# Optimization experiments

Measured on AMD Instinct MI355X. Metric: run time of the kernel, lower is better.

## Reference

```python
import jax, jax.numpy as jnp
import numpy as np

N_NODES = 100000
N_EDGES = 1600000
D_FEAT = 256
HIDDEN = 256
OUT = 128


def _glorot(key, shape):
    fan_in, fan_out = shape[1], shape[0]
    lim = float(np.sqrt(6.0 / (fan_in + fan_out)))
    return jax.random.uniform(key, shape, jnp.float32, -lim, lim)


def setup_inputs() -> dict:
    key = jax.random.key(0)
    ks = jax.random.split(key, 12)
    x = jax.random.normal(ks[0], (N_NODES, D_FEAT), jnp.float32)
    edge_index = jax.random.randint(ks[1], (2, N_EDGES), 0, N_NODES, jnp.int64)
    return {
        "x": x,
        "edge_index": edge_index,
        # SAGEConv1: lin_l (neighbors, has bias), lin_r (root, no bias)
        "W1l": _glorot(ks[2], (HIDDEN, D_FEAT)),
        "b1l": jnp.zeros((HIDDEN,), jnp.float32),
        "W1r": _glorot(ks[3], (HIDDEN, D_FEAT)),
        # SAGEConv2
        "W2l": _glorot(ks[4], (OUT, HIDDEN)),
        "b2l": jnp.zeros((OUT,), jnp.float32),
        "W2r": _glorot(ks[5], (OUT, HIDDEN)),
        # EdgeDecoder
        "Wd1": _glorot(ks[6], (OUT, 2 * OUT)),
        "bd1": jnp.zeros((OUT,), jnp.float32),
        "Wd2": _glorot(ks[7], (1, OUT)),
        "bd2": jnp.zeros((1,), jnp.float32),
    }


def _sage_conv(x, src, dst, Wl, bl, Wr):
    # mean-aggregate source features into destination nodes (PyG SAGEConv, aggr='mean')
    msg_sum = jax.ops.segment_sum(x[src], dst, num_segments=N_NODES)  # [N, d]
    cnt = jax.ops.segment_sum(jnp.ones((src.shape[0],), x.dtype), dst, num_segments=N_NODES)
    mean = msg_sum / jnp.maximum(cnt, 1.0)[:, None]
    return mean @ Wl.T + bl + x @ Wr.T


def reference(x, edge_index, W1l, b1l, W1r, W2l, b2l, W2r, Wd1, bd1, Wd2, bd2):
    src, dst = edge_index[0], edge_index[1]
    # NodeEncoder
    h = jax.nn.relu(_sage_conv(x, src, dst, W1l, b1l, W1r))
    z = _sage_conv(h, src, dst, W2l, b2l, W2r)  # [N, OUT]
    # EdgeDecoder: gather per-edge endpoint embeddings, concat, MLP
    zc = jnp.concatenate([z[src], z[dst]], axis=-1)  # [E, 2*OUT]
    hd = jax.nn.relu(zc @ Wd1.T + bd1)
    out = hd @ Wd2.T + bd2  # [E, 1]
    return out.reshape(-1)
```

## Files before the change

kernel.cpp:

```cpp
#include <hip/hip_runtime.h>
#include <stdint.h>

static constexpr int NN = 100000;
static constexpr int NE = 1600000;
static constexpr int NB_SCAN = (NN + 255) / 256;
static constexpr int NB_CVTX = NN * 256 / 4 / 256;
static constexpr int NB_HIST = NE / 256;
static constexpr int NB_CVTW = 897;

typedef __bf16 bf16;
typedef __bf16 bf16x4 __attribute__((ext_vector_type(4)));
typedef __bf16 bf16x8 __attribute__((ext_vector_type(8)));
typedef float floatx4 __attribute__((ext_vector_type(4)));

__device__ __forceinline__ void async16(const void* g, void* l) {
  __builtin_amdgcn_global_load_lds(
      (const __attribute__((address_space(1))) void*)g,
      (__attribute__((address_space(3))) void*)l, 16, 0, 0);
}

__device__ __forceinline__ uint32_t pk4_fp8(float a, float b, float c, float d) {
  uint32_t v = 0;
  v = (uint32_t)__builtin_amdgcn_cvt_pk_fp8_f32(a, b, (int)v, false);
  v = (uint32_t)__builtin_amdgcn_cvt_pk_fp8_f32(c, d, (int)v, true);
  return v;
}

__device__ __forceinline__ void acc_fp8x8(float* a, uint2 v) {
  a[0] += __builtin_amdgcn_cvt_f32_fp8(v.x, 0);
  a[1] += __builtin_amdgcn_cvt_f32_fp8(v.x, 1);
  a[2] += __builtin_amdgcn_cvt_f32_fp8(v.x, 2);
  a[3] += __builtin_amdgcn_cvt_f32_fp8(v.x, 3);
  a[4] += __builtin_amdgcn_cvt_f32_fp8(v.y, 0);
  a[5] += __builtin_amdgcn_cvt_f32_fp8(v.y, 1);
  a[6] += __builtin_amdgcn_cvt_f32_fp8(v.y, 2);
  a[7] += __builtin_amdgcn_cvt_f32_fp8(v.y, 3);
}

__device__ __forceinline__ int clampN(int c) {
  return ((unsigned)c < (unsigned)NN) ? c : 0;
}

__global__ void k_cvtx_hist(const float* __restrict__ x, bf16* __restrict__ xb,
                            uint32_t* __restrict__ xq,
                            const int* __restrict__ dst, int* __restrict__ cnt8,
                            uint16_t* __restrict__ rank) {
  int b = blockIdx.x;
  int m = b % 5;
  if (m < 4) {
    int cb = (b / 5) * 4 + m;
    int t = cb * 256 + threadIdx.x;
    const float4 v = ((const float4*)x)[t];
    bf16x4 o;
    o.x = (bf16)v.x; o.y = (bf16)v.y; o.z = (bf16)v.z; o.w = (bf16)v.w;
    ((bf16x4*)xb)[t] = o;
    xq[t] = pk4_fp8(v.x, v.y, v.z, v.w);
  } else {
    int hb = b / 5;
    int e = hb * 256 + threadIdx.x;
    uint32_t xcd;
    asm("s_getreg_b32 %0, hwreg(HW_REG_XCC_ID)" : "=s"(xcd));
    xcd &= 7u;
    int d = dst[e];
    int old = __hip_atomic_fetch_add(&cnt8[(size_t)xcd * NN + d], 1,
                                     __ATOMIC_RELAXED, __HIP_MEMORY_SCOPE_WORKGROUP);
    rank[e] = (uint16_t)((xcd << 12) | ((uint32_t)old & 0xFFFu));
  }
}

__global__ void k_cvtw_scanpart(
    const float* __restrict__ W1l, const float* __restrict__ W1r,
    const float* __restrict__ W2l, const float* __restrict__ W2r,
    const float* __restrict__ Wd1, const float* __restrict__ bd1,
    bf16* __restrict__ B1, bf16* __restrict__ B2,
    bf16* __restrict__ Bd, float* __restrict__ biasPQ,
    const int* __restrict__ cnt8, int* __restrict__ part, int N) {
  int b = blockIdx.x;
  if (b < NB_CVTW) {
    int g = b * 256 + threadIdx.x;
    if (g < 131072) {
      int o = g >> 9, k = g & 511;
      float v = (k < 256) ? W1l[o * 256 + k] : W1r[o * 256 + k - 256];
      B1[g] = (bf16)v;
    } else if (g < 131072 + 65536) {
      int t = g - 131072;
      int o = t >> 8, k = t & 255;
      float v = (o < 128) ? W2l[o * 256 + k] : W2r[(o - 128) * 256 + k];
      B2[t] = (bf16)v;
    } else if (g < 131072 + 65536 + 32768) {
      int t = g - 196608;
      int o = t >> 7, k = t & 127;
      float v = (o < 128) ? Wd1[o * 256 + k] : Wd1[(o - 128) * 256 + 128 + k];
      Bd[t] = (bf16)v;
    } else if (g < 131072 + 65536 + 32768 + 256) {
      int t = g - 229376;
      biasPQ[t] = (t < 128) ? bd1[t] : 0.0f;
    }
  } else {
    __shared__ int sh[256];
    int bb = b - NB_CVTW;
    int t = threadIdx.x;
    int i = bb * 256 + t;
    int tot = 0;
    if (i < N) {
#pragma unroll
      for (int xx = 0; xx < 8; ++xx) tot += cnt8[(size_t)xx * NN + i];
    }
    sh[t] = tot;
    __syncthreads();
    for (int off = 128; off > 0; off >>= 1) {
      if (t < off) sh[t] += sh[t + off];
      __syncthreads();
    }
    if (t == 0) part[bb] = sh[0];
  }
}

__global__ __launch_bounds__(512) void k_scan_mid(int* __restrict__ part, int NB) {
  __shared__ int sh[512];
  int t = threadIdx.x;
  int v = (t < NB) ? part[t] : 0;
  sh[t] = v;
  __syncthreads();
  for (int off = 1; off < 512; off <<= 1) {
    int u = (t >= off) ? sh[t - off] : 0;
    __syncthreads();
    sh[t] += u;
    __syncthreads();
  }
  if (t < NB) part[t] = sh[t] - v;
}

__global__ void k_scan_fin(int* __restrict__ cnt8, const int* __restrict__ part,
                           int* __restrict__ rowptr, int N, int E) {
  __shared__ int sh[256];
  int t = threadIdx.x;
  int i = blockIdx.x * 256 + t;
  int c[8];
  int v = 0;
  if (i < N) {
#pragma unroll
    for (int xx = 0; xx < 8; ++xx) { c[xx] = cnt8[(size_t)xx * NN + i]; v += c[xx]; }
  } else {
#pragma unroll
    for (int xx = 0; xx < 8; ++xx) c[xx] = 0;
  }
  sh[t] = v;
  __syncthreads();
  for (int off = 1; off < 256; off <<= 1) {
    int u = (t >= off) ? sh[t - off] : 0;
    __syncthreads();
    sh[t] += u;
    __syncthreads();
  }
  if (i < N) {
    int base = part[blockIdx.x] + sh[t] - v;
    rowptr[i] = base;
#pragma unroll
    for (int xx = 0; xx < 8; ++xx) { cnt8[(size_t)xx * NN + i] = base; base += c[xx]; }
  }
  if (i == 0) rowptr[N] = E;
}

__global__ void k_fill(const int* __restrict__ src, const int* __restrict__ dst,
                       const int* __restrict__ rptr8,
                       const uint16_t* __restrict__ rank,
                       int* __restrict__ csr, int E) {
  int e = blockIdx.x * 256 + threadIdx.x;
  if (e < E) {
    int d = dst[e];
    uint32_t rv = rank[e];
    int pos = rptr8[(size_t)(rv >> 12) * NN + d] + (int)(rv & 0xFFFu);
    if ((unsigned)pos >= (unsigned)E) pos = 0;
    csr[pos] = src[e];
  }
}

__global__ void k_agg(const uint8_t* __restrict__ xq, const int* __restrict__ rowptr,
                      const int* __restrict__ csr, bf16* __restrict__ mean) {
  int wave = threadIdx.x >> 6, lane = threadIdx.x & 63;
  int n = blockIdx.x * 4 + wave;
  int s = rowptr[n], e = rowptr[n + 1];
  int half = lane >> 5, l32 = lane & 31;
  float a[8] = {};
  const uint8_t* base = xq + l32 * 8;
  int i = s + half;
  for (; i + 6 < e; i += 8) {
    int c0 = clampN(csr[i]), c1 = clampN(csr[i + 2]);
    int c2 = clampN(csr[i + 4]), c3 = clampN(csr[i + 6]);
    uint2 v0 = *(const uint2*)(base + (size_t)c0 * 256);
    uint2 v1 = *(const uint2*)(base + (size_t)c1 * 256);
    uint2 v2 = *(const uint2*)(base + (size_t)c2 * 256);
    uint2 v3 = *(const uint2*)(base + (size_t)c3 * 256);
    acc_fp8x8(a, v0); acc_fp8x8(a, v1); acc_fp8x8(a, v2); acc_fp8x8(a, v3);
  }
  for (; i < e; i += 2) {
    uint2 v = *(const uint2*)(base + (size_t)clampN(csr[i]) * 256);
    acc_fp8x8(a, v);
  }
  int deg = e - s;
  float sc = 1.0f / (float)(deg > 0 ? deg : 1);
  bf16x8 o;
#pragma unroll
  for (int j = 0; j < 8; ++j) {
    float t = a[j] + __shfl_xor(a[j], 32);
    o[j] = (bf16)(t * sc);
  }
  if (half == 0)
    *(bf16x8*)(mean + (size_t)n * 256 + l32 * 8) = o;
}

__global__ void k_agg2z(const uint8_t* __restrict__ hq, const bf16* __restrict__ hr,
                        const int* __restrict__ rowptr, const int* __restrict__ csr,
                        const float* __restrict__ b2l, bf16* __restrict__ zf) {
  int wave = threadIdx.x >> 6, lane = threadIdx.x & 63;
  int n = blockIdx.x * 4 + wave;
  int s = rowptr[n], e = rowptr[n + 1];
  int sub = lane >> 4, l16 = lane & 15;
  float a[8] = {};
  const uint8_t* base = hq + l16 * 8;
  int i = s + sub;
  for (; i + 4 < e; i += 8) {
    int c0 = clampN(csr[i]), c1 = clampN(csr[i + 4]);
    uint2 v0 = *(const uint2*)(base + (size_t)c0 * 128);
    uint2 v1 = *(const uint2*)(base + (size_t)c1 * 128);
    acc_fp8x8(a, v0); acc_fp8x8(a, v1);
  }
  for (; i < e; i += 4) {
    uint2 v = *(const uint2*)(base + (size_t)clampN(csr[i]) * 128);
    acc_fp8x8(a, v);
  }
  int deg = e - s;
  float sc = 1.0f / (float)(deg > 0 ? deg : 1);
  bf16x8 hv = *(const bf16x8*)(hr + (size_t)n * 128 + l16 * 8);
  const float4* b4 = (const float4*)(b2l + l16 * 8);
  float4 ba = b4[0], bb = b4[1];
  float bl[8] = {ba.x, ba.y, ba.z, ba.w, bb.x, bb.y, bb.z, bb.w};
  bf16x8 o;
#pragma unroll
  for (int j = 0; j < 8; ++j) {
    float t = a[j];
    t += __shfl_xor(t, 16);
    t += __shfl_xor(t, 32);
    o[j] = (bf16)(t * sc + (float)hv[j] + bl[j]);
  }
  if (sub == 0)
    *(bf16x8*)(zf + (size_t)n * 128 + l16 * 8) = o;
}

__global__ __launch_bounds__(256) void k_conv_gemm(
    const bf16* __restrict__ A1, const bf16* __restrict__ A2,
    const bf16* __restrict__ B, const float* __restrict__ bias,
    bf16* __restrict__ out, int Nrows) {
  __shared__ bf16 As[128 * 64];
  __shared__ bf16 Bs[128 * 64];
  const int tid = threadIdx.x, wave = tid >> 6, lane = tid & 63;
  const int quad = lane >> 4, l16 = lane & 15;
  const int rowBase = blockIdx.y * 128;
  const int colBase = blockIdx.x * 128;
  const int wr = (wave >> 1) * 64;
  const int wc = (wave & 1) * 64;
  floatx4 acc[4][4] = {};

  for (int kc = 0; kc < 8; ++kc) {
    const bf16* Asrc = (kc < 4) ? A1 : A2;
    const int kb = (kc & 3) * 64;
    for (int i = 0; i < 4; ++i) {
      int u = wave * 256 + i * 64 + lane;
      int row = u >> 3, seg = u & 7;
      int sg = seg ^ (row & 7);
      int node = rowBase + row;
      if (node >= Nrows) node = Nrows - 1;
      async16(Asrc + (size_t)node * 256 + kb + sg * 8, &As[(wave * 256 + i * 64) * 8]);
    }
    for (int i = 0; i < 4; ++i) {
      int u = wave * 256 + i * 64 + lane;
      int row = u >> 3, seg = u & 7;
      int sg = seg ^ (row & 7);
      async16(B + (size_t)(colBase + row) * 512 + kc * 64 + sg * 8,
              &Bs[(wave * 256 + i * 64) * 8]);
    }
    __syncthreads();
    for (int ks = 0; ks < 2; ++ks) {
      bf16x8 af[4], bq[4];
      const int sw = (ks * 4 + quad) ^ (l16 & 7);
      for (int mt = 0; mt < 4; ++mt)
        af[mt] = *(const bf16x8*)&As[(wr + mt * 16 + l16) * 64 + sw * 8];
      for (int nt = 0; nt < 4; ++nt)
        bq[nt] = *(const bf16x8*)&Bs[(wc + nt * 16 + l16) * 64 + sw * 8];
      for (int mt = 0; mt < 4; ++mt)
        for (int nt = 0; nt < 4; ++nt)
          acc[mt][nt] = __builtin_amdgcn_mfma_f32_16x16x32_bf16(af[mt], bq[nt], acc[mt][nt], 0, 0, 0);
    }
    __syncthreads();
  }
  float bv[4];
  for (int nt = 0; nt < 4; ++nt) bv[nt] = bias[colBase + wc + nt * 16 + l16];
  for (int mt = 0; mt < 4; ++mt)
    for (int nt = 0; nt < 4; ++nt) {
      int gcol = colBase + wc + nt * 16 + l16;
      for (int r = 0; r < 4; ++r) {
        int grow = rowBase + wr + mt * 16 + quad * 4 + r;
        if (grow < Nrows) {
          float v = fmaxf(acc[mt][nt][r] + bv[nt], 0.0f);
          out[(size_t)grow * 256 + gcol] = (bf16)v;
        }
      }
    }
}

template <int KDIM, int EPI>
__global__ __launch_bounds__(256) void k_gemm(
    const bf16* __restrict__ A, const bf16* __restrict__ B,
    const float* __restrict__ bias, void* __restrict__ out1,
    void* __restrict__ out2, int Nrows) {
  __shared__ bf16 As[128 * 64];
  __shared__ bf16 Bs[128 * 64];
  const int tid = threadIdx.x, wave = tid >> 6, lane = tid & 63;
  const int quad = lane >> 4, l16 = lane & 15;
  const int rowBase = blockIdx.y * 128;
  const int colBase = blockIdx.x * 128;
  const int wr = (wave >> 1) * 64;
  const int wc = (wave & 1) * 64;
  floatx4 acc[4][4] = {};

  for (int kc = 0; kc < KDIM / 64; ++kc) {
    for (int i = 0; i < 4; ++i) {
      int u = wave * 256 + i * 64 + lane;
      int row = u >> 3, seg = u & 7;
      int sg = seg ^ (row & 7);
      int node = rowBase + row;
      if (node >= Nrows) node = Nrows - 1;
      async16(A + (size_t)node * KDIM + kc * 64 + sg * 8, &As[(wave * 256 + i * 64) * 8]);
    }
    for (int i = 0; i < 4; ++i) {
      int u = wave * 256 + i * 64 + lane;
      int row = u >> 3, seg = u & 7;
      int sg = seg ^ (row & 7);
      async16(B + (size_t)(colBase + row) * KDIM + kc * 64 + sg * 8,
              &Bs[(wave * 256 + i * 64) * 8]);
    }
    __syncthreads();
    for (int ks = 0; ks < 2; ++ks) {
      bf16x8 af[4], bq[4];
      const int sw = (ks * 4 + quad) ^ (l16 & 7);
      for (int mt = 0; mt < 4; ++mt)
        af[mt] = *(const bf16x8*)&As[(wr + mt * 16 + l16) * 64 + sw * 8];
      for (int nt = 0; nt < 4; ++nt)
        bq[nt] = *(const bf16x8*)&Bs[(wc + nt * 16 + l16) * 64 + sw * 8];
      for (int mt = 0; mt < 4; ++mt)
        for (int nt = 0; nt < 4; ++nt)
          acc[mt][nt] = __builtin_amdgcn_mfma_f32_16x16x32_bf16(af[mt], bq[nt], acc[mt][nt], 0, 0, 0);
    }
    __syncthreads();
  }
  float bv[4];
  for (int nt = 0; nt < 4; ++nt)
    bv[nt] = (EPI == 2) ? bias[colBase + wc + nt * 16 + l16] : 0.0f;
  const bool lowHalf = (colBase == 0);
  for (int mt = 0; mt < 4; ++mt)
    for (int nt = 0; nt < 4; ++nt) {
      int gcol = colBase + wc + nt * 16 + l16;
      for (int r = 0; r < 4; ++r) {
        int grow = rowBase + wr + mt * 16 + quad * 4 + r;
        if (grow < Nrows) {
          float v = acc[mt][nt][r] + bv[nt];
          if (lowHalf) {
            if (EPI == 1) {
              uint32_t pk = (uint32_t)__builtin_amdgcn_cvt_pk_fp8_f32(v, v, 0, false);
              ((uint8_t*)out1)[(size_t)grow * 128 + gcol] = (uint8_t)pk;
            } else {
              ((bf16*)out1)[(size_t)grow * 128 + gcol] = (bf16)v;
            }
          } else {
            ((bf16*)out2)[(size_t)grow * 128 + gcol - 128] = (bf16)v;
          }
        }
      }
    }
}

__global__ __launch_bounds__(256) void k_edge(
    const bf16* __restrict__ P, const bf16* __restrict__ Q,
    const int* __restrict__ rowptr, const int* __restrict__ csr,
    const float* __restrict__ wd2, const float* __restrict__ bd2,
    float* __restrict__ outCSR) {
  int wave = threadIdx.x >> 6, lane = threadIdx.x & 63;
  int n = blockIdx.x * 4 + wave;
  int s = rowptr[n], e = rowptr[n + 1];
  int sub = lane >> 4, l16 = lane & 15;
  bf16x8 qv = *(const bf16x8*)(Q + (size_t)n * 128 + l16 * 8);
  float qf[8];
#pragma unroll
  for (int j = 0; j < 8; ++j) qf[j] = (float)qv[j];
  const float4* w4 = (const float4*)(wd2 + l16 * 8);
  float4 wa = w4[0], wb = w4[1];
  float w[8] = {wa.x, wa.y, wa.z, wa.w, wb.x, wb.y, wb.z, wb.w};
  const float bout = bd2[0];
  int i = s + sub;
  for (; i + 4 < e; i += 8) {
    int c0 = clampN(csr[i]), c1 = clampN(csr[i + 4]);
    bf16x8 p0 = *(const bf16x8*)(P + (size_t)c0 * 128 + l16 * 8);
    bf16x8 p1 = *(const bf16x8*)(P + (size_t)c1 * 128 + l16 * 8);
    float a0 = 0.f, a1 = 0.f;
#pragma unroll
    for (int j = 0; j < 8; ++j) {
      a0 += fmaxf((float)p0[j] + qf[j], 0.f) * w[j];
      a1 += fmaxf((float)p1[j] + qf[j], 0.f) * w[j];
    }
    a0 += __shfl_xor(a0, 1); a1 += __shfl_xor(a1, 1);
    a0 += __shfl_xor(a0, 2); a1 += __shfl_xor(a1, 2);
    a0 += __shfl_xor(a0, 4); a1 += __shfl_xor(a1, 4);
    a0 += __shfl_xor(a0, 8); a1 += __shfl_xor(a1, 8);
    if (l16 == 0) { outCSR[i] = a0 + bout; outCSR[i + 4] = a1 + bout; }
  }
  for (; i < e; i += 4) {
    int c = clampN(csr[i]);
    bf16x8 p = *(const bf16x8*)(P + (size_t)c * 128 + l16 * 8);
    float a = 0.f;
#pragma unroll
    for (int j = 0; j < 8; ++j)
      a += fmaxf((float)p[j] + qf[j], 0.f) * w[j];
    a += __shfl_xor(a, 1);
    a += __shfl_xor(a, 2);
    a += __shfl_xor(a, 4);
    a += __shfl_xor(a, 8);
    if (l16 == 0) outCSR[i] = a + bout;
  }
}

__global__ void k_perm(const int* __restrict__ dst, const uint16_t* __restrict__ rank,
                       const int* __restrict__ rptr8, const float* __restrict__ outCSR,
                       float* __restrict__ out, int E) {
  int e = blockIdx.x * 256 + threadIdx.x;
  if (e < E) {
    int d = dst[e];
    uint32_t rv = rank[e];
    int pos = rptr8[(size_t)(rv >> 12) * NN + d] + (int)(rv & 0xFFFu);
    if ((unsigned)pos >= (unsigned)E) pos = 0;
    out[e] = outCSR[pos];
  }
}

extern "C" void kernel_launch(void* const* d_in, const int* in_sizes, int n_in,
                              void* d_out, int out_size, void* d_ws, size_t ws_size,
                              hipStream_t stream) {
  const float* x   = (const float*)d_in[0];
  const int*   ei  = (const int*)d_in[1];
  const float* W1l = (const float*)d_in[2];
  const float* b1l = (const float*)d_in[3];
  const float* W1r = (const float*)d_in[4];
  const float* W2l = (const float*)d_in[5];
  const float* b2l = (const float*)d_in[6];
  const float* W2r = (const float*)d_in[7];
  const float* Wd1 = (const float*)d_in[8];
  const float* bd1 = (const float*)d_in[9];
  const float* Wd2 = (const float*)d_in[10];
  const float* bd2 = (const float*)d_in[11];
  float* out = (float*)d_out;

  const int N = NN, E = NE;
  const int* srcv = ei;
  const int* dstv = ei + E;

  char* w = (char*)d_ws;
  size_t off = 0;
  auto take = [&](size_t bytes) {
    size_t o = off;
    off = (off + bytes + 255) & ~(size_t)255;
    return o;
  };
  int*      cnt8   = (int*)(w + take((size_t)8 * N * 4));
  int*      rowptr = (int*)(w + take((size_t)(N + 1) * 4));
  int*      part   = (int*)(w + take((size_t)NB_SCAN * 4));
  uint16_t* rank   = (uint16_t*)(w + take((size_t)E * 2));
  int*      csr    = (int*)(w + take((size_t)E * 4));
  bf16*     xb     = (bf16*)(w + take((size_t)N * 256 * 2));
  uint8_t*  xq     = (uint8_t*)(w + take((size_t)N * 256));
  bf16*     mean   = (bf16*)(w + take((size_t)N * 256 * 2));
  bf16*     h      = (bf16*)(w + take((size_t)N * 256 * 2));
  bf16*     zf     = (bf16*)(w + take((size_t)N * 128 * 2));
  bf16*     B1     = (bf16*)(w + take((size_t)131072 * 2));
  bf16*     B2     = (bf16*)(w + take((size_t)65536 * 2));
  bf16*     Bd     = (bf16*)(w + take((size_t)32768 * 2));
  float*    biasPQ = (float*)(w + take((size_t)256 * 4));
  int*     rptr8 = cnt8;
  float*   outCSR = (float*)xb;
  uint8_t* hq = (uint8_t*)mean;
  bf16*    hr = (bf16*)(hq + (size_t)N * 128);
  bf16*    P  = h;
  bf16*    Q  = h + (size_t)N * 128;
  (void)ws_size; (void)n_in; (void)in_sizes; (void)out_size;

  hipMemsetAsync(cnt8, 0, (size_t)8 * N * 4, stream);

  k_cvtx_hist<<<NB_CVTX + NB_HIST, 256, 0, stream>>>(x, xb, (uint32_t*)xq, dstv, cnt8, rank);
  k_cvtw_scanpart<<<NB_CVTW + NB_SCAN, 256, 0, stream>>>(
      W1l, W1r, W2l, W2r, Wd1, bd1, B1, B2, Bd, biasPQ, cnt8, part, N);
  k_scan_mid<<<1, 512, 0, stream>>>(part, NB_SCAN);
  k_scan_fin<<<NB_SCAN, 256, 0, stream>>>(cnt8, part, rowptr, N, E);
  k_fill<<<E / 256, 256, 0, stream>>>(srcv, dstv, rptr8, rank, csr, E);

  k_agg<<<N / 4, 256, 0, stream>>>(xq, rowptr, csr, mean);
  k_conv_gemm<<<dim3(2, 782), 256, 0, stream>>>(mean, xb, B1, b1l, h, N);
  k_gemm<256, 1><<<dim3(2, 782), 256, 0, stream>>>(h, B2, nullptr, hq, hr, N);
  k_agg2z<<<N / 4, 256, 0, stream>>>(hq, hr, rowptr, csr, b2l, zf);
  k_gemm<128, 2><<<dim3(2, 782), 256, 0, stream>>>(zf, Bd, biasPQ, P, Q, N);
  k_edge<<<N / 4, 256, 0, stream>>>(P, Q, rowptr, csr, Wd2, bd2, outCSR);
  k_perm<<<E / 256, 256, 0, stream>>>(dstv, rank, rptr8, outCSR, out, E);
}
```

Before: 577.3 us.

## Fuse layer-1 conv GEMM with layer-2 projection GEMM through LDS-resident hidden tile

Merges the first SAGE conv GEMM and the second layer's projection GEMM into one 512-thread kernel. Each block computes a full 128x256 hidden tile, applies bias and ReLU, keeps it in swizzled LDS, then multiplies by B2 to emit the fp8 aggregation input and the bf16 root term. This removes the global write and re-read of the hidden activations and one launch. In exchange it uses about 112 KB of LDS per block and a 512-thread block, so occupancy drops and there is less parallelism (782 blocks instead of 1564). Buffer aliases are reassigned so hq/hr live in h and P/Q live in mean.

```diff
diff --git a/kernel.cpp b/kernel.cpp
--- a/kernel.cpp
+++ b/kernel.cpp
@@ -248,37 +248,37 @@
     *(bf16x8*)(zf + (size_t)n * 128 + l16 * 8) = o;
 }
 
-__global__ __launch_bounds__(256) void k_conv_gemm(
+__global__ __launch_bounds__(512) void k_fused12(
     const bf16* __restrict__ A1, const bf16* __restrict__ A2,
-    const bf16* __restrict__ B, const float* __restrict__ bias,
-    bf16* __restrict__ out, int Nrows) {
+    const bf16* __restrict__ B1, const float* __restrict__ b1l,
+    const bf16* __restrict__ B2, uint8_t* __restrict__ hq,
+    bf16* __restrict__ hr, int Nrows) {
+  __shared__ bf16 Hs[128 * 256];
   __shared__ bf16 As[128 * 64];
-  __shared__ bf16 Bs[128 * 64];
+  __shared__ bf16 Bs[256 * 64];
   const int tid = threadIdx.x, wave = tid >> 6, lane = tid & 63;
   const int quad = lane >> 4, l16 = lane & 15;
-  const int rowBase = blockIdx.y * 128;
-  const int colBase = blockIdx.x * 128;
-  const int wr = (wave >> 1) * 64;
-  const int wc = (wave & 1) * 64;
+  const int rowBase = blockIdx.x * 128;
+  const int wr = (wave >> 2) * 64;
+  const int wc = (wave & 3) * 64;
   floatx4 acc[4][4] = {};
 
   for (int kc = 0; kc < 8; ++kc) {
     const bf16* Asrc = (kc < 4) ? A1 : A2;
     const int kb = (kc & 3) * 64;
+    for (int i = 0; i < 2; ++i) {
+      int u = wave * 128 + i * 64 + lane;
+      int row = u >> 3, seg = u & 7;
+      int sg = seg ^ (row & 7);
+      int node = rowBase + row;
+      if (node >= Nrows) node = Nrows - 1;
+      async16(Asrc + (size_t)node * 256 + kb + sg * 8, &As[(wave * 128 + i * 64) * 8]);
+    }
     for (int i = 0; i < 4; ++i) {
       int u = wave * 256 + i * 64 + lane;
       int row = u >> 3, seg = u & 7;
       int sg = seg ^ (row & 7);
-      int node = rowBase + row;
-      if (node >= Nrows) node = Nrows - 1;
-      async16(Asrc + (size_t)node * 256 + kb + sg * 8, &As[(wave * 256 + i * 64) * 8]);
-    }
-    for (int i = 0; i < 4; ++i) {
-      int u = wave * 256 + i * 64 + lane;
-      int row = u >> 3, seg = u & 7;
-      int sg = seg ^ (row & 7);
-      async16(B + (size_t)(colBase + row) * 512 + kc * 64 + sg * 8,
-              &Bs[(wave * 256 + i * 64) * 8]);
+      async16(B1 + (size_t)row * 512 + kc * 64 + sg * 8, &Bs[(wave * 256 + i * 64) * 8]);
     }
     __syncthreads();
     for (int ks = 0; ks < 2; ++ks) {
@@ -294,16 +294,62 @@
     }
     __syncthreads();
   }
-  float bv[4];
-  for (int nt = 0; nt < 4; ++nt) bv[nt] = bias[colBase + wc + nt * 16 + l16];
+
+  {
+    float bv1[4];
+    for (int nt = 0; nt < 4; ++nt) bv1[nt] = b1l[wc + nt * 16 + l16];
+    for (int mt = 0; mt < 4; ++mt)
+      for (int nt = 0; nt < 4; ++nt) {
+        int col = wc + nt * 16 + l16;
+        int c = col >> 3;
+        for (int r = 0; r < 4; ++r) {
+          int row = wr + mt * 16 + quad * 4 + r;
+          float v = fmaxf(acc[mt][nt][r] + bv1[nt], 0.0f);
+          Hs[row * 256 + (c ^ (row & 7)) * 8 + (col & 7)] = (bf16)v;
+          acc[mt][nt][r] = 0.0f;
+        }
+      }
+  }
+  __syncthreads();
+
+  for (int kc = 0; kc < 4; ++kc) {
+    for (int i = 0; i < 4; ++i) {
+      int u = wave * 256 + i * 64 + lane;
+      int row = u >> 3, seg = u & 7;
+      int sg = seg ^ (row & 7);
+      async16(B2 + (size_t)row * 256 + kc * 64 + sg * 8, &Bs[(wave * 256 + i * 64) * 8]);
+    }
+    __syncthreads();
+    for (int ks = 0; ks < 2; ++ks) {
+      bf16x8 af[4], bq[4];
+      const int swb = (ks * 4 + quad) ^ (l16 & 7);
+      const int ck = kc * 8 + ks * 4 + quad;
+      for (int mt = 0; mt < 4; ++mt) {
+        int row = wr + mt * 16 + l16;
+        af[mt] = *(const bf16x8*)&Hs[row * 256 + (ck ^ (row & 7)) * 8];
+      }
+      for (int nt = 0; nt < 4; ++nt)
+        bq[nt] = *(const bf16x8*)&Bs[(wc + nt * 16 + l16) * 64 + swb * 8];
+      for (int mt = 0; mt < 4; ++mt)
+        for (int nt = 0; nt < 4; ++nt)
+          acc[mt][nt] = __builtin_amdgcn_mfma_f32_16x16x32_bf16(af[mt], bq[nt], acc[mt][nt], 0, 0, 0);
+    }
+    __syncthreads();
+  }
+
   for (int mt = 0; mt < 4; ++mt)
     for (int nt = 0; nt < 4; ++nt) {
-      int gcol = colBase + wc + nt * 16 + l16;
+      int oc = wc + nt * 16 + l16;
       for (int r = 0; r < 4; ++r) {
         int grow = rowBase + wr + mt * 16 + quad * 4 + r;
         if (grow < Nrows) {
-          float v = fmaxf(acc[mt][nt][r] + bv[nt], 0.0f);
-          out[(size_t)grow * 256 + gcol] = (bf16)v;
+          float v = acc[mt][nt][r];
+          if (oc < 128) {
+            uint32_t pk = (uint32_t)__builtin_amdgcn_cvt_pk_fp8_f32(v, v, 0, false);
+            hq[(size_t)grow * 128 + oc] = (uint8_t)pk;
+          } else {
+            hr[(size_t)grow * 128 + oc - 128] = (bf16)v;
+          }
         }
       }
     }
@@ -486,10 +532,10 @@
   float*    biasPQ = (float*)(w + take((size_t)256 * 4));
   int*     rptr8 = cnt8;
   float*   outCSR = (float*)xb;
-  uint8_t* hq = (uint8_t*)mean;
+  uint8_t* hq = (uint8_t*)h;
   bf16*    hr = (bf16*)(hq + (size_t)N * 128);
-  bf16*    P  = h;
-  bf16*    Q  = h + (size_t)N * 128;
+  bf16*    P  = mean;
+  bf16*    Q  = mean + (size_t)N * 128;
   (void)ws_size; (void)n_in; (void)in_sizes; (void)out_size;
 
   hipMemsetAsync(cnt8, 0, (size_t)8 * N * 4, stream);
@@ -502,8 +548,7 @@
   k_fill<<<E / 256, 256, 0, stream>>>(srcv, dstv, rptr8, rank, csr, E);
 
   k_agg<<<N / 4, 256, 0, stream>>>(xq, rowptr, csr, mean);
-  k_conv_gemm<<<dim3(2, 782), 256, 0, stream>>>(mean, xb, B1, b1l, h, N);
-  k_gemm<256, 1><<<dim3(2, 782), 256, 0, stream>>>(h, B2, nullptr, hq, hr, N);
+  k_fused12<<<782, 512, 0, stream>>>(mean, xb, B1, b1l, B2, hq, hr, N);
   k_agg2z<<<N / 4, 256, 0, stream>>>(hq, hr, rowptr, csr, b2l, zf);
   k_gemm<128, 2><<<dim3(2, 782), 256, 0, stream>>>(zf, Bd, biasPQ, P, Q, N);
   k_edge<<<N / 4, 256, 0, stream>>>(P, Q, rowptr, csr, Wd2, bd2, outCSR);
```

New measurement: 570.8 us. No clear change (-1.1%).
